# Kernel optimization log

Measured on AMD Instinct MI355X. Metric: run time of the kernel, lower is better.

The kernel has to match this reference:

```python
import jax, jax.numpy as jnp
import numpy as np

N, E, L, S = 20000, 100000, 128, 6   # nodes, edges, latent, message-passing steps
NF, EF, TW, OUT = 11, 5, 5, 1        # node feat, edge feat, time_window, output_size
LN_EPS = 1e-5


def _mlp_ln(x, W1, b1, W2, b2, g, beta):
    # Linear -> ReLU -> Linear -> ReLU -> LayerNorm (matches torch Sequential)
    h = jax.nn.relu(x @ W1 + b1)
    h = jax.nn.relu(h @ W2 + b2)
    mu = h.mean(-1, keepdims=True)
    var = ((h - mu) ** 2).mean(-1, keepdims=True)
    return (h - mu) * jax.lax.rsqrt(var + LN_EPS) * g + beta


def setup_inputs() -> dict:
    key = jax.random.key(0)
    ks = iter(jax.random.split(key, 64))

    def w(shape):
        fan_in = shape[-2]
        return jax.random.normal(next(ks), shape, jnp.float32) / np.float32(np.sqrt(fan_in))

    inp = {
        'node_features': jax.random.normal(next(ks), (1, N, NF), jnp.float32),
        'edge_features': jax.random.normal(next(ks), (1, E, EF), jnp.float32),
        'senders': jax.random.randint(next(ks), (E,), 0, N, jnp.int32),
        'receivers': jax.random.randint(next(ks), (E,), 0, N, jnp.int32),
        'node_mean': jax.random.normal(next(ks), (NF,), jnp.float32),
        'node_std': jnp.ones((NF,), jnp.float32),
        'edge_mean': jax.random.normal(next(ks), (EF,), jnp.float32),
        'edge_std': jnp.ones((EF,), jnp.float32),
        'enc_n_W1': w((NF, L)), 'enc_n_b1': jnp.zeros((L,), jnp.float32),
        'enc_n_W2': w((L, L)), 'enc_n_b2': jnp.zeros((L,), jnp.float32),
        'enc_n_g': jnp.ones((L,), jnp.float32), 'enc_n_beta': jnp.zeros((L,), jnp.float32),
        'enc_e_W1': w((EF, L)), 'enc_e_b1': jnp.zeros((L,), jnp.float32),
        'enc_e_W2': w((L, L)), 'enc_e_b2': jnp.zeros((L,), jnp.float32),
        'enc_e_g': jnp.ones((L,), jnp.float32), 'enc_e_beta': jnp.zeros((L,), jnp.float32),
        'blk_e_W1': w((S, 3 * L, L)), 'blk_e_b1': jnp.zeros((S, L), jnp.float32),
        'blk_e_W2': w((S, L, L)), 'blk_e_b2': jnp.zeros((S, L), jnp.float32),
        'blk_e_g': jnp.ones((S, L), jnp.float32), 'blk_e_beta': jnp.zeros((S, L), jnp.float32),
        'blk_n_W1': w((S, 2 * L, L)), 'blk_n_b1': jnp.zeros((S, L), jnp.float32),
        'blk_n_W2': w((S, L, L)), 'blk_n_b2': jnp.zeros((S, L), jnp.float32),
        'blk_n_g': jnp.ones((S, L), jnp.float32), 'blk_n_beta': jnp.zeros((S, L), jnp.float32),
        'dec_W1': w((L, 8)), 'dec_b1': jnp.zeros((8,), jnp.float32),
        'dec_W2': w((8, TW)), 'dec_b2': jnp.zeros((TW,), jnp.float32),
    }
    return inp


def reference(node_features, edge_features, senders, receivers,
              node_mean, node_std, edge_mean, edge_std,
              enc_n_W1, enc_n_b1, enc_n_W2, enc_n_b2, enc_n_g, enc_n_beta,
              enc_e_W1, enc_e_b1, enc_e_W2, enc_e_b2, enc_e_g, enc_e_beta,
              blk_e_W1, blk_e_b1, blk_e_W2, blk_e_b2, blk_e_g, blk_e_beta,
              blk_n_W1, blk_n_b1, blk_n_W2, blk_n_b2, blk_n_g, blk_n_beta,
              dec_W1, dec_b1, dec_W2, dec_b2):
    # ---- encode (Normalizer in eval mode: (x - mean) / std) ----
    node_lat = _mlp_ln((node_features - node_mean) / node_std,
                       enc_n_W1, enc_n_b1, enc_n_W2, enc_n_b2, enc_n_g, enc_n_beta)  # [1,N,L]
    edge_lat = _mlp_ln((edge_features - edge_mean) / edge_std,
                       enc_e_W1, enc_e_b1, enc_e_W2, enc_e_b2, enc_e_g, enc_e_beta)  # [1,E,L]

    # ---- process: gather -> edge MLP -> scatter_add -> node MLP, residuals ----
    for i in range(S):
        e_in = jnp.concatenate([node_lat[:, senders, :], node_lat[:, receivers, :], edge_lat], axis=-1)  # [1,E,3L]
        new_e = _mlp_ln(e_in, blk_e_W1[i], blk_e_b1[i], blk_e_W2[i], blk_e_b2[i], blk_e_g[i], blk_e_beta[i])
        aggr = jax.ops.segment_sum(new_e[0], receivers, num_segments=N)[None]  # [1,N,L]
        new_n = _mlp_ln(jnp.concatenate([node_lat, aggr], axis=-1),
                        blk_n_W1[i], blk_n_b1[i], blk_n_W2[i], blk_n_b2[i], blk_n_g[i], blk_n_beta[i])
        node_lat = node_lat + new_n
        edge_lat = edge_lat + new_e

    # ---- decode: Conv1d(k=1) == per-node linear; Swish(beta=1) ----
    h = node_lat[0] @ dec_W1 + dec_b1          # [N,8]
    h = h * jax.nn.sigmoid(h)
    dec = h @ dec_W2 + dec_b2                  # [N,TW]
    dt = jnp.repeat(jnp.arange(1, TW + 1), OUT).astype(dec.dtype)  # [TW*OUT]
    delta = (dec * dt).reshape(N, TW, OUT).transpose(1, 0, 2)      # [TW,N,OUT]
    return delta
```

## Files before the change

kernel.cpp:

```cpp
#include <hip/hip_runtime.h>
#include <cstdint>
#include <cstddef>


#define N_NODES 20000
#define N_EDGES 100000
#define LDIM    128
#define NSTEPS  6

typedef float  f32x4  __attribute__((ext_vector_type(4)));
typedef __bf16 bf16x8 __attribute__((ext_vector_type(8)));
typedef __bf16 bf16x2 __attribute__((ext_vector_type(2)));

__device__ __forceinline__ bf16x8 cvt8(const float* p) {
  float4 u = *(const float4*)p;
  float4 v = *(const float4*)(p + 4);
  bf16x8 o;
  o[0] = (__bf16)u.x; o[1] = (__bf16)u.y; o[2] = (__bf16)u.z; o[3] = (__bf16)u.w;
  o[4] = (__bf16)v.x; o[5] = (__bf16)v.y; o[6] = (__bf16)v.z; o[7] = (__bf16)v.w;
  return o;
}

struct PrepArgs {
  const float *s_enW1, *s_enW2, *s_eeW1, *s_eeW2;
  const float *s_beW1, *s_beW2, *s_bnW1, *s_bnW2;
  __bf16 *d_enW1, *d_enW2, *d_eeW1, *d_eeW2;
  __bf16 *d_beW1, *d_beW2, *d_bnW1, *d_bnW2;
  int* counts;
};

__device__ __forceinline__ void swz_src(int idx, int& k, int& col) {
  int j    = idx & 7;
  int lane = (idx >> 3) & 63;
  int ct   = (idx >> 9) & 7;
  int kc   = idx >> 12;
  col = ct * 16 + (lane & 15);
  k   = kc * 32 + (lane >> 4) * 8 + j;
}

__global__ __launch_bounds__(256) void prep_kernel(PrepArgs p) {
  int idx = blockIdx.x * 256 + threadIdx.x;
  int k, col;

  if (idx < 4096) {
    swz_src(idx, k, col);
    p.d_enW1[idx] = (__bf16)((k < 11) ? p.s_enW1[k * 128 + col] : 0.f);
    return;
  }
  idx -= 4096;
  if (idx < 16384) {
    swz_src(idx, k, col);
    p.d_enW2[idx] = (__bf16)p.s_enW2[k * 128 + col];
    return;
  }
  idx -= 16384;
  if (idx < 4096) {
    swz_src(idx, k, col);
    p.d_eeW1[idx] = (__bf16)((k < 5) ? p.s_eeW1[k * 128 + col] : 0.f);
    return;
  }
  idx -= 4096;
  if (idx < 16384) {
    swz_src(idx, k, col);
    p.d_eeW2[idx] = (__bf16)p.s_eeW2[k * 128 + col];
    return;
  }
  idx -= 16384;
  if (idx < 294912) {
    int s = idx / 49152, rem = idx % 49152;
    swz_src(rem, k, col);
    p.d_beW1[idx] = (__bf16)p.s_beW1[(size_t)s * 49152 + k * 128 + col];
    return;
  }
  idx -= 294912;
  if (idx < 98304) {
    int s = idx >> 14, rem = idx & 16383;
    swz_src(rem, k, col);
    p.d_beW2[idx] = (__bf16)p.s_beW2[s * 16384 + k * 128 + col];
    return;
  }
  idx -= 98304;
  if (idx < 196608) {
    int s = idx >> 15, rem = idx & 32767;
    swz_src(rem, k, col);
    p.d_bnW1[idx] = (__bf16)p.s_bnW1[s * 32768 + k * 128 + col];
    return;
  }
  idx -= 196608;
  if (idx < 98304) {
    int s = idx >> 14, rem = idx & 16383;
    swz_src(rem, k, col);
    p.d_bnW2[idx] = (__bf16)p.s_bnW2[s * 16384 + k * 128 + col];
    return;
  }
  idx -= 98304;
  if (idx < N_NODES) p.counts[idx] = 0;
}

__global__ __launch_bounds__(256) void hist_kernel(const int* __restrict__ recv,
                                                   int* __restrict__ counts) {
  int e = blockIdx.x * 256 + threadIdx.x;
  if (e < N_EDGES) atomicAdd(&counts[recv[e]], 1);
}

__global__ __launch_bounds__(1024) void scan_kernel(const int* __restrict__ counts,
                                                    int* __restrict__ row_ptr,
                                                    int* __restrict__ cursor) {
  __shared__ int part[1024];
  const int t = threadIdx.x;
  const int base = t * 20;
  int local[20];
  int s = 0;
#pragma unroll
  for (int i = 0; i < 20; ++i) {
    int idx = base + i;
    int v = (idx < N_NODES) ? counts[idx] : 0;
    local[i] = s;
    s += v;
  }
  part[t] = s;
  __syncthreads();
  for (int off = 1; off < 1024; off <<= 1) {
    int add = (t >= off) ? part[t - off] : 0;
    __syncthreads();
    part[t] += add;
    __syncthreads();
  }
  const int excl = part[t] - s;
#pragma unroll
  for (int i = 0; i < 20; ++i) {
    int idx = base + i;
    if (idx < N_NODES) {
      int v = excl + local[i];
      row_ptr[idx] = v;
      cursor[idx]  = v;
    }
  }
  if (t == 1023) row_ptr[N_NODES] = part[1023];
}

__global__ __launch_bounds__(256) void fill_kernel(const int* __restrict__ recv,
                                                   int* __restrict__ cursor,
                                                   int* __restrict__ edge_list) {
  int e = blockIdx.x * 256 + threadIdx.x;
  if (e < N_EDGES) {
    int r = recv[e];
    int pos = atomicAdd(&cursor[r], 1);
    edge_list[pos] = e;
  }
}

__global__ __launch_bounds__(256) void agg_kernel(
    const int* __restrict__ row_ptr, const int* __restrict__ edge_list,
    const __bf16* __restrict__ new_e, __bf16* __restrict__ aggr_bf) {
  const int wv   = threadIdx.x >> 6;
  const int lane = threadIdx.x & 63;
  const int n    = blockIdx.x * 4 + wv;
  if (n >= N_NODES) return;
  int p = row_ptr[n];
  const int pe = row_ptr[n + 1];
  float s0 = 0.f, s1 = 0.f;
  while (p < pe) {
    const int cnt = min(pe - p, 64);
    int eid = (lane < cnt) ? edge_list[p + lane] : 0;
    for (int j = 0; j < cnt; ++j) {
      const int e = __shfl(eid, j);
      bf16x2 v = *(const bf16x2*)(new_e + (size_t)e * LDIM + lane * 2);
      s0 += (float)v[0];
      s1 += (float)v[1];
    }
    p += cnt;
  }
  bf16x2 o;
  o[0] = (__bf16)s0; o[1] = (__bf16)s1;
  *(bf16x2*)(aggr_bf + (size_t)n * LDIM + lane * 2) = o;
}

struct MlpArgs {
  const float* x; const float* mean; const float* stdv;
  float* node_lat; float* edge_lat;
  __bf16* new_e;
  const __bf16* aggr_bf;
  __bf16* node_bf;
  const int* senders; const int* receivers;
  const __bf16* W1t; const __bf16* W2t;
  const float* b1; const float* b2; const float* g; const float* beta;
  int M;
};

template <int K1, int MODE>
__global__ __launch_bounds__(64, 3) void mlp2_kernel(MlpArgs a) {
  constexpr int NKC = K1 / 32;
  constexpr int RT  = 2;
  constexpr int HS  = 136;

  __shared__ __align__(16) __bf16 H1[32 * HS];

  const int lane  = threadIdx.x & 63;
  const int l15   = lane & 15;
  const int quad  = lane >> 4;
  const int M     = a.M;
  const int rbase = blockIdx.x * 32;

  __bf16* h1w = H1;

  int rowA[RT];
#pragma unroll
  for (int rt = 0; rt < RT; ++rt) {
    int r = rbase + rt * 16 + l15;
    rowA[rt] = (r < M) ? r : (M - 1);
  }

  int sA[RT], rA[RT];
  if constexpr (MODE == 2) {
#pragma unroll
    for (int rt = 0; rt < RT; ++rt) {
      sA[rt] = a.senders[rowA[rt]];
      rA[rt] = a.receivers[rowA[rt]];
    }
  }

  f32x4 acc[RT][8];
#pragma unroll
  for (int rt = 0; rt < RT; ++rt)
#pragma unroll
    for (int i = 0; i < 8; ++i) acc[rt][i] = (f32x4)(0.f);

  if constexpr (MODE == 0 || MODE == 1) {
    constexpr int KIN = (MODE == 0) ? 11 : 5;
    bf16x8 af[RT];
#pragma unroll
    for (int rt = 0; rt < RT; ++rt) {
      const float* xr = a.x + (size_t)rowA[rt] * KIN;
#pragma unroll
      for (int j = 0; j < 8; ++j) {
        int c = quad * 8 + j;
        float v = (c < KIN) ? (xr[c] - a.mean[c]) / a.stdv[c] : 0.f;
        af[rt][j] = (__bf16)v;
      }
    }
    bf16x8 bfv[8];
#pragma unroll
    for (int ct = 0; ct < 8; ++ct)
      bfv[ct] = *(const bf16x8*)(a.W1t + (ct * 64 + lane) * 8);
#pragma unroll
    for (int rt = 0; rt < RT; ++rt)
#pragma unroll
      for (int ct = 0; ct < 8; ++ct)
        acc[rt][ct] = __builtin_amdgcn_mfma_f32_16x16x32_bf16(af[rt], bfv[ct], acc[rt][ct], 0, 0, 0);
  } else {
    constexpr int NPH = NKC / 4;
#pragma unroll
    for (int ph = 0; ph < NPH; ++ph) {
      bf16x8 afr[RT][4];
#pragma unroll
      for (int kk = 0; kk < 4; ++kk) {
#pragma unroll
        for (int rt = 0; rt < RT; ++rt) {
          if constexpr (MODE == 2) {
            if (ph == 0)
              afr[rt][kk] = *(const bf16x8*)(a.node_bf + (size_t)sA[rt] * LDIM + kk * 32 + quad * 8);
            else if (ph == 1)
              afr[rt][kk] = *(const bf16x8*)(a.node_bf + (size_t)rA[rt] * LDIM + kk * 32 + quad * 8);
            else
              afr[rt][kk] = cvt8(a.edge_lat + (size_t)rowA[rt] * LDIM + kk * 32 + quad * 8);
          } else {
            if (ph == 0)
              afr[rt][kk] = *(const bf16x8*)(a.node_bf + (size_t)rowA[rt] * LDIM + kk * 32 + quad * 8);
            else
              afr[rt][kk] = *(const bf16x8*)(a.aggr_bf + (size_t)rowA[rt] * LDIM + kk * 32 + quad * 8);
          }
        }
      }
#pragma unroll
      for (int kk = 0; kk < 4; ++kk) {
        const int kc = ph * 4 + kk;
        bf16x8 bfv[8];
#pragma unroll
        for (int ct = 0; ct < 8; ++ct)
          bfv[ct] = *(const bf16x8*)(a.W1t + ((kc * 8 + ct) * 64 + lane) * 8);
#pragma unroll
        for (int rt = 0; rt < RT; ++rt)
#pragma unroll
          for (int ct = 0; ct < 8; ++ct)
            acc[rt][ct] = __builtin_amdgcn_mfma_f32_16x16x32_bf16(afr[rt][kk], bfv[ct], acc[rt][ct], 0, 0, 0);
      }
    }
  }

#pragma unroll
  for (int ct = 0; ct < 8; ++ct) {
    const float bb = a.b1[ct * 16 + l15];
#pragma unroll
    for (int rt = 0; rt < RT; ++rt)
#pragma unroll
      for (int rr = 0; rr < 4; ++rr) {
        float v = fmaxf(acc[rt][ct][rr] + bb, 0.f);
        h1w[(rt * 16 + quad * 4 + rr) * HS + ct * 16 + l15] = (__bf16)v;
      }
  }

#pragma unroll
  for (int rt = 0; rt < RT; ++rt)
#pragma unroll
    for (int i = 0; i < 8; ++i) acc[rt][i] = (f32x4)(0.f);

#pragma unroll
  for (int kc = 0; kc < 4; ++kc) {
    bf16x8 af[RT];
#pragma unroll
    for (int rt = 0; rt < RT; ++rt)
      af[rt] = *(const bf16x8*)(h1w + (rt * 16 + l15) * HS + kc * 32 + quad * 8);
    bf16x8 bfv[8];
#pragma unroll
    for (int ct = 0; ct < 8; ++ct)
      bfv[ct] = *(const bf16x8*)(a.W2t + ((kc * 8 + ct) * 64 + lane) * 8);
#pragma unroll
    for (int rt = 0; rt < RT; ++rt)
#pragma unroll
      for (int ct = 0; ct < 8; ++ct)
        acc[rt][ct] = __builtin_amdgcn_mfma_f32_16x16x32_bf16(af[rt], bfv[ct], acc[rt][ct], 0, 0, 0);
  }

#pragma unroll
  for (int ct = 0; ct < 8; ++ct) {
    const float bb = a.b2[ct * 16 + l15];
#pragma unroll
    for (int rt = 0; rt < RT; ++rt)
#pragma unroll
      for (int rr = 0; rr < 4; ++rr)
        acc[rt][ct][rr] = fmaxf(acc[rt][ct][rr] + bb, 0.f);
  }

  float mu[RT][4], rs[RT][4];
#pragma unroll
  for (int rt = 0; rt < RT; ++rt)
#pragma unroll
    for (int rr = 0; rr < 4; ++rr) {
      float s = 0.f, s2 = 0.f;
#pragma unroll
      for (int ct = 0; ct < 8; ++ct) { float v = acc[rt][ct][rr]; s += v; s2 += v * v; }
      s  += __shfl_xor(s, 1);  s2 += __shfl_xor(s2, 1);
      s  += __shfl_xor(s, 2);  s2 += __shfl_xor(s2, 2);
      s  += __shfl_xor(s, 4);  s2 += __shfl_xor(s2, 4);
      s  += __shfl_xor(s, 8);  s2 += __shfl_xor(s2, 8);
      float m = s * (1.f / 128.f);
      float var = fmaxf(s2 * (1.f / 128.f) - m * m, 0.f);
      mu[rt][rr] = m; rs[rt][rr] = rsqrtf(var + 1e-5f);
    }

  float gv[8], bev[8];
#pragma unroll
  for (int ct = 0; ct < 8; ++ct) {
    gv[ct]  = a.g[ct * 16 + l15];
    bev[ct] = a.beta[ct * 16 + l15];
  }

#pragma unroll
  for (int rt = 0; rt < RT; ++rt)
#pragma unroll
    for (int rr = 0; rr < 4; ++rr) {
      const int row = rbase + rt * 16 + quad * 4 + rr;
      if (row >= M) continue;
      if constexpr (MODE == 2) {
#pragma unroll
        for (int ct = 0; ct < 8; ++ct) {
          const int col = ct * 16 + l15;
          float y = (acc[rt][ct][rr] - mu[rt][rr]) * rs[rt][rr] * gv[ct] + bev[ct];
          a.edge_lat[(size_t)row * LDIM + col] += y;
          a.new_e[(size_t)row * LDIM + col] = (__bf16)y;
        }
      } else if constexpr (MODE == 3) {
#pragma unroll
        for (int ct = 0; ct < 8; ++ct) {
          const int col = ct * 16 + l15;
          float y = (acc[rt][ct][rr] - mu[rt][rr]) * rs[rt][rr] * gv[ct] + bev[ct];
          float nv = a.node_lat[(size_t)row * LDIM + col] + y;
          a.node_lat[(size_t)row * LDIM + col] = nv;
          a.node_bf[(size_t)row * LDIM + col] = (__bf16)nv;
        }
      } else if constexpr (MODE == 0) {
#pragma unroll
        for (int ct = 0; ct < 8; ++ct) {
          const int col = ct * 16 + l15;
          float y = (acc[rt][ct][rr] - mu[rt][rr]) * rs[rt][rr] * gv[ct] + bev[ct];
          a.node_lat[(size_t)row * LDIM + col] = y;
          a.node_bf[(size_t)row * LDIM + col] = (__bf16)y;
        }
      } else {
#pragma unroll
        for (int ct = 0; ct < 8; ++ct) {
          const int col = ct * 16 + l15;
          float y = (acc[rt][ct][rr] - mu[rt][rr]) * rs[rt][rr] * gv[ct] + bev[ct];
          a.edge_lat[(size_t)row * LDIM + col] = y;
        }
      }
    }
}

__global__ __launch_bounds__(256) void decode_kernel(
    const float* __restrict__ node_lat,
    const float* __restrict__ W1, const float* __restrict__ b1,
    const float* __restrict__ W2, const float* __restrict__ b2,
    float* __restrict__ out) {
  __shared__ float X[64][129];
  const int n0 = blockIdx.x * 64;
  for (int idx = threadIdx.x; idx < 64 * 32; idx += 256) {
    int r = idx >> 5, c4 = idx & 31;
    int n = n0 + r; if (n >= N_NODES) n = N_NODES - 1;
    float4 v = *((const float4*)(node_lat + (size_t)n * 128) + c4);
    X[r][c4 * 4 + 0] = v.x; X[r][c4 * 4 + 1] = v.y;
    X[r][c4 * 4 + 2] = v.z; X[r][c4 * 4 + 3] = v.w;
  }
  __syncthreads();
  const int r = threadIdx.x;
  if (r < 64) {
    const int n = n0 + r;
    if (n < N_NODES) {
      float h[8];
#pragma unroll
      for (int j = 0; j < 8; ++j) h[j] = b1[j];
      for (int k = 0; k < 128; ++k) {
        float xv = X[r][k];
#pragma unroll
        for (int j = 0; j < 8; ++j) h[j] = fmaf(xv, W1[k * 8 + j], h[j]);
      }
#pragma unroll
      for (int j = 0; j < 8; ++j) h[j] = h[j] / (1.f + expf(-h[j]));
#pragma unroll
      for (int t = 0; t < 5; ++t) {
        float d = b2[t];
#pragma unroll
        for (int j = 0; j < 8; ++j) d = fmaf(h[j], W2[j * 5 + t], d);
        out[t * N_NODES + n] = d * (float)(t + 1);
      }
    }
  }
}

extern "C" void kernel_launch(void* const* d_in, const int* in_sizes, int n_in,
                              void* d_out, int out_size, void* d_ws, size_t ws_size,
                              hipStream_t stream) {
  (void)in_sizes; (void)n_in; (void)out_size; (void)ws_size;

  const float* node_features = (const float*)d_in[0];
  const float* edge_features = (const float*)d_in[1];
  const int*   senders       = (const int*)d_in[2];
  const int*   receivers     = (const int*)d_in[3];
  const float* node_mean = (const float*)d_in[4];
  const float* node_std  = (const float*)d_in[5];
  const float* edge_mean = (const float*)d_in[6];
  const float* edge_std  = (const float*)d_in[7];
  const float* enc_n_W1 = (const float*)d_in[8];
  const float* enc_n_b1 = (const float*)d_in[9];
  const float* enc_n_W2 = (const float*)d_in[10];
  const float* enc_n_b2 = (const float*)d_in[11];
  const float* enc_n_g    = (const float*)d_in[12];
  const float* enc_n_beta = (const float*)d_in[13];
  const float* enc_e_W1 = (const float*)d_in[14];
  const float* enc_e_b1 = (const float*)d_in[15];
  const float* enc_e_W2 = (const float*)d_in[16];
  const float* enc_e_b2 = (const float*)d_in[17];
  const float* enc_e_g    = (const float*)d_in[18];
  const float* enc_e_beta = (const float*)d_in[19];
  const float* blk_e_W1 = (const float*)d_in[20];
  const float* blk_e_b1 = (const float*)d_in[21];
  const float* blk_e_W2 = (const float*)d_in[22];
  const float* blk_e_b2 = (const float*)d_in[23];
  const float* blk_e_g    = (const float*)d_in[24];
  const float* blk_e_beta = (const float*)d_in[25];
  const float* blk_n_W1 = (const float*)d_in[26];
  const float* blk_n_b1 = (const float*)d_in[27];
  const float* blk_n_W2 = (const float*)d_in[28];
  const float* blk_n_b2 = (const float*)d_in[29];
  const float* blk_n_g    = (const float*)d_in[30];
  const float* blk_n_beta = (const float*)d_in[31];
  const float* dec_W1 = (const float*)d_in[32];
  const float* dec_b1 = (const float*)d_in[33];
  const float* dec_W2 = (const float*)d_in[34];
  const float* dec_b2 = (const float*)d_in[35];

  char* ws = (char*)d_ws;
  float*  node_lat = (float*)(ws);
  float*  edge_lat = (float*)(ws + 10240000);
  __bf16* new_e    = (__bf16*)(ws + 61440000);
  __bf16* wb       = (__bf16*)(ws + 87040000);
  int* counts    = (int*)(ws + 88498176);
  int* row_ptr   = (int*)(ws + 88578176);
  int* cursor    = (int*)(ws + 88658192);
  int* edge_list = (int*)(ws + 88738192);
  __bf16* aggr_bf = (__bf16*)(ws + 89138192);
  __bf16* node_bf = (__bf16*)(ws + 94258192);

  __bf16* enW1s = wb;
  __bf16* enW2s = enW1s + 4096;
  __bf16* eeW1s = enW2s + 16384;
  __bf16* eeW2s = eeW1s + 4096;
  __bf16* beW1s = eeW2s + 16384;
  __bf16* beW2s = beW1s + 6 * 49152;
  __bf16* bnW1s = beW2s + 6 * 16384;
  __bf16* bnW2s = bnW1s + 6 * 32768;

  PrepArgs pa;
  pa.s_enW1 = enc_n_W1; pa.s_enW2 = enc_n_W2; pa.s_eeW1 = enc_e_W1; pa.s_eeW2 = enc_e_W2;
  pa.s_beW1 = blk_e_W1; pa.s_beW2 = blk_e_W2; pa.s_bnW1 = blk_n_W1; pa.s_bnW2 = blk_n_W2;
  pa.d_enW1 = enW1s; pa.d_enW2 = enW2s; pa.d_eeW1 = eeW1s; pa.d_eeW2 = eeW2s;
  pa.d_beW1 = beW1s; pa.d_beW2 = beW2s; pa.d_bnW1 = bnW1s; pa.d_bnW2 = bnW2s;
  pa.counts = counts;
  prep_kernel<<<2927, 256, 0, stream>>>(pa);

  hist_kernel<<<(N_EDGES + 255) / 256, 256, 0, stream>>>(receivers, counts);
  scan_kernel<<<1, 1024, 0, stream>>>(counts, row_ptr, cursor);
  fill_kernel<<<(N_EDGES + 255) / 256, 256, 0, stream>>>(receivers, cursor, edge_list);

  const int NODE_BLOCKS = (N_NODES + 31) / 32;
  const int EDGE_BLOCKS = (N_EDGES + 31) / 32;
  const int DEC_BLOCKS  = (N_NODES + 63) / 64;
  const int AGG_BLOCKS  = (N_NODES + 3) / 4;

  MlpArgs base;
  base.node_lat = node_lat; base.edge_lat = edge_lat; base.new_e = new_e;
  base.aggr_bf = aggr_bf; base.node_bf = node_bf;
  base.senders = senders; base.receivers = receivers;
  base.x = nullptr; base.mean = nullptr; base.stdv = nullptr;

  {
    MlpArgs a = base;
    a.x = node_features; a.mean = node_mean; a.stdv = node_std;
    a.W1t = enW1s; a.W2t = enW2s;
    a.b1 = enc_n_b1; a.b2 = enc_n_b2; a.g = enc_n_g; a.beta = enc_n_beta;
    a.M = N_NODES;
    mlp2_kernel<32, 0><<<NODE_BLOCKS, 64, 0, stream>>>(a);
  }
  {
    MlpArgs a = base;
    a.x = edge_features; a.mean = edge_mean; a.stdv = edge_std;
    a.W1t = eeW1s; a.W2t = eeW2s;
    a.b1 = enc_e_b1; a.b2 = enc_e_b2; a.g = enc_e_g; a.beta = enc_e_beta;
    a.M = N_EDGES;
    mlp2_kernel<32, 1><<<EDGE_BLOCKS, 64, 0, stream>>>(a);
  }

  for (int i = 0; i < NSTEPS; ++i) {
    {
      MlpArgs a = base;
      a.W1t = beW1s + (size_t)i * 49152; a.W2t = beW2s + (size_t)i * 16384;
      a.b1 = blk_e_b1 + i * 128; a.b2 = blk_e_b2 + i * 128;
      a.g = blk_e_g + i * 128; a.beta = blk_e_beta + i * 128;
      a.M = N_EDGES;
      mlp2_kernel<384, 2><<<EDGE_BLOCKS, 64, 0, stream>>>(a);
    }
    agg_kernel<<<AGG_BLOCKS, 256, 0, stream>>>(row_ptr, edge_list, new_e, aggr_bf);
    {
      MlpArgs a = base;
      a.W1t = bnW1s + (size_t)i * 32768; a.W2t = bnW2s + (size_t)i * 16384;
      a.b1 = blk_n_b1 + i * 128; a.b2 = blk_n_b2 + i * 128;
      a.g = blk_n_g + i * 128; a.beta = blk_n_beta + i * 128;
      a.M = N_NODES;
      mlp2_kernel<256, 3><<<NODE_BLOCKS, 64, 0, stream>>>(a);
    }
  }

  decode_kernel<<<DEC_BLOCKS, 256, 0, stream>>>(
      node_lat, dec_W1, dec_b1, dec_W2, dec_b2, (float*)d_out);
}
```

Before: 705.3 us.

## Precompute per-node sender/receiver projections before edge MLP gather

Splits the edge MLP's first layer so that the sender and receiver slices of W1 are applied once per node by a new projection kernel into an fp32 buffer P. The edge kernel then gathers the projected rows, adds the edge-latent matmul and bias, and applies ReLU, which cuts the per-edge first-layer MFMA work by two thirds. In exchange it gathers fp32 256-wide rows instead of bf16 128-wide rows, staging goes through fp32 shared memory, and each step adds a kernel launch. It also skips the edge_lat residual update on the last step, since that value is never read afterwards.

Measured after the change: 867.1 us. +22.9%, slower.

```diff
diff --git a/kernel.cpp b/kernel.cpp
--- a/kernel.cpp
+++ b/kernel.cpp
@@ -26,6 +26,7 @@
   const float *s_beW1, *s_beW2, *s_bnW1, *s_bnW2;
   __bf16 *d_enW1, *d_enW2, *d_eeW1, *d_eeW2;
   __bf16 *d_beW1, *d_beW2, *d_bnW1, *d_bnW2;
+  __bf16 *d_Wp;
   int* counts;
 };
 
@@ -94,6 +95,21 @@
     return;
   }
   idx -= 98304;
+  if (idx < 196608) {
+    int s = idx >> 15, rem = idx & 32767;
+    int j    = rem & 7;
+    int lane = (rem >> 3) & 63;
+    int ct   = (rem >> 9) & 15;
+    int kc   = rem >> 13;
+    int outcol = ct * 16 + (lane & 15);
+    int kk = kc * 32 + (lane >> 4) * 8 + j;
+    float v = (outcol < 128)
+        ? p.s_beW1[(size_t)s * 49152 + kk * 128 + outcol]
+        : p.s_beW1[(size_t)s * 49152 + (128 + kk) * 128 + (outcol - 128)];
+    p.d_Wp[idx] = (__bf16)v;
+    return;
+  }
+  idx -= 196608;
   if (idx < N_NODES) p.counts[idx] = 0;
 }
 
@@ -176,16 +192,54 @@
   *(bf16x2*)(aggr_bf + (size_t)n * LDIM + lane * 2) = o;
 }
 
+__global__ __launch_bounds__(64, 4) void proj_kernel(
+    const __bf16* __restrict__ node_bf, const __bf16* __restrict__ Wp,
+    float* __restrict__ P) {
+  const int lane = threadIdx.x & 63;
+  const int l15  = lane & 15;
+  const int quad = lane >> 4;
+  const int rbase = blockIdx.x * 16;
+  int row = rbase + l15; if (row >= N_NODES) row = N_NODES - 1;
+
+  bf16x8 af[4];
+#pragma unroll
+  for (int kc = 0; kc < 4; ++kc)
+    af[kc] = *(const bf16x8*)(node_bf + (size_t)row * LDIM + kc * 32 + quad * 8);
+
+  f32x4 acc[16];
+#pragma unroll
+  for (int i = 0; i < 16; ++i) acc[i] = (f32x4)(0.f);
+
+#pragma unroll
+  for (int kc = 0; kc < 4; ++kc)
+#pragma unroll
+    for (int ct = 0; ct < 16; ++ct) {
+      bf16x8 b = *(const bf16x8*)(Wp + ((kc * 16 + ct) * 64 + lane) * 8);
+      acc[ct] = __builtin_amdgcn_mfma_f32_16x16x32_bf16(af[kc], b, acc[ct], 0, 0, 0);
+    }
+
+#pragma unroll
+  for (int ct = 0; ct < 16; ++ct)
+#pragma unroll
+    for (int rr = 0; rr < 4; ++rr) {
+      int r2 = rbase + quad * 4 + rr;
+      if (r2 < N_NODES)
+        P[(size_t)r2 * 256 + ct * 16 + l15] = acc[ct][rr];
+    }
+}
+
 struct MlpArgs {
   const float* x; const float* mean; const float* stdv;
   float* node_lat; float* edge_lat;
   __bf16* new_e;
   const __bf16* aggr_bf;
   __bf16* node_bf;
+  const float* P;
   const int* senders; const int* receivers;
   const __bf16* W1t; const __bf16* W2t;
   const float* b1; const float* b2; const float* g; const float* beta;
   int M;
+  int write_elat;
 };
 
 template <int K1, int MODE>
@@ -193,8 +247,10 @@
   constexpr int NKC = K1 / 32;
   constexpr int RT  = 2;
   constexpr int HS  = 136;
-
-  __shared__ __align__(16) __bf16 H1[32 * HS];
+  constexpr int FS  = 132;
+  constexpr int SMB = (MODE == 2) ? (32 * FS * 4) : (32 * HS * 2);
+
+  __shared__ __align__(16) char SMEM[SMB];
 
   const int lane  = threadIdx.x & 63;
   const int l15   = lane & 15;
@@ -202,8 +258,6 @@
   const int M     = a.M;
   const int rbase = blockIdx.x * 32;
 
-  __bf16* h1w = H1;
-
   int rowA[RT];
 #pragma unroll
   for (int rt = 0; rt < RT; ++rt) {
@@ -226,100 +280,168 @@
 #pragma unroll
     for (int i = 0; i < 8; ++i) acc[rt][i] = (f32x4)(0.f);
 
-  if constexpr (MODE == 0 || MODE == 1) {
-    constexpr int KIN = (MODE == 0) ? 11 : 5;
-    bf16x8 af[RT];
+  if constexpr (MODE == 2) {
+    float* SP = (float*)SMEM;
+    bf16x8 afr[RT][4];
+#pragma unroll
+    for (int kk = 0; kk < 4; ++kk)
+#pragma unroll
+      for (int rt = 0; rt < RT; ++rt)
+        afr[rt][kk] = cvt8(a.edge_lat + (size_t)rowA[rt] * LDIM + kk * 32 + quad * 8);
+#pragma unroll
+    for (int kk = 0; kk < 4; ++kk) {
+      bf16x8 bfv[8];
+#pragma unroll
+      for (int ct = 0; ct < 8; ++ct)
+        bfv[ct] = *(const bf16x8*)(a.W1t + (((kk + 8) * 8 + ct) * 64 + lane) * 8);
+#pragma unroll
+      for (int rt = 0; rt < RT; ++rt)
+#pragma unroll
+        for (int ct = 0; ct < 8; ++ct)
+          acc[rt][ct] = __builtin_amdgcn_mfma_f32_16x16x32_bf16(afr[rt][kk], bfv[ct], acc[rt][ct], 0, 0, 0);
+    }
+#pragma unroll
+    for (int ct = 0; ct < 8; ++ct)
+#pragma unroll
+      for (int rt = 0; rt < RT; ++rt)
+#pragma unroll
+        for (int rr = 0; rr < 4; ++rr)
+          SP[(rt * 16 + quad * 4 + rr) * FS + ct * 16 + l15] = acc[rt][ct][rr];
+
 #pragma unroll
     for (int rt = 0; rt < RT; ++rt) {
-      const float* xr = a.x + (size_t)rowA[rt] * KIN;
-#pragma unroll
-      for (int j = 0; j < 8; ++j) {
-        int c = quad * 8 + j;
-        float v = (c < KIN) ? (xr[c] - a.mean[c]) / a.stdv[c] : 0.f;
-        af[rt][j] = (__bf16)v;
+      const float* Ps = a.P + (size_t)sA[rt] * 256;
+      const float* Pr = a.P + (size_t)rA[rt] * 256 + 128;
+      float* spr = SP + (rt * 16 + l15) * FS;
+#pragma unroll
+      for (int kk = 0; kk < 4; ++kk) {
+        const int c0 = kk * 32 + quad * 8;
+        float4 a0 = *(const float4*)(Ps + c0);
+        float4 a1 = *(const float4*)(Ps + c0 + 4);
+        float4 b0 = *(const float4*)(Pr + c0);
+        float4 b1v = *(const float4*)(Pr + c0 + 4);
+        float4 g0 = *(const float4*)(a.b1 + c0);
+        float4 g1 = *(const float4*)(a.b1 + c0 + 4);
+        float4 c0v = *(const float4*)(spr + c0);
+        float4 c1v = *(const float4*)(spr + c0 + 4);
+        c0v.x = fmaxf(c0v.x + a0.x + b0.x + g0.x, 0.f);
+        c0v.y = fmaxf(c0v.y + a0.y + b0.y + g0.y, 0.f);
+        c0v.z = fmaxf(c0v.z + a0.z + b0.z + g0.z, 0.f);
+        c0v.w = fmaxf(c0v.w + a0.w + b0.w + g0.w, 0.f);
+        c1v.x = fmaxf(c1v.x + a1.x + b1v.x + g1.x, 0.f);
+        c1v.y = fmaxf(c1v.y + a1.y + b1v.y + g1.y, 0.f);
+        c1v.z = fmaxf(c1v.z + a1.z + b1v.z + g1.z, 0.f);
+        c1v.w = fmaxf(c1v.w + a1.w + b1v.w + g1.w, 0.f);
+        *(float4*)(spr + c0)     = c0v;
+        *(float4*)(spr + c0 + 4) = c1v;
       }
     }
-    bf16x8 bfv[8];
-#pragma unroll
-    for (int ct = 0; ct < 8; ++ct)
-      bfv[ct] = *(const bf16x8*)(a.W1t + (ct * 64 + lane) * 8);
+
 #pragma unroll
     for (int rt = 0; rt < RT; ++rt)
 #pragma unroll
+      for (int i = 0; i < 8; ++i) acc[rt][i] = (f32x4)(0.f);
+#pragma unroll
+    for (int kc = 0; kc < 4; ++kc) {
+      bf16x8 af2[RT];
+#pragma unroll
+      for (int rt = 0; rt < RT; ++rt)
+        af2[rt] = cvt8(SP + (rt * 16 + l15) * FS + kc * 32 + quad * 8);
+      bf16x8 bfv[8];
+#pragma unroll
       for (int ct = 0; ct < 8; ++ct)
-        acc[rt][ct] = __builtin_amdgcn_mfma_f32_16x16x32_bf16(af[rt], bfv[ct], acc[rt][ct], 0, 0, 0);
+        bfv[ct] = *(const bf16x8*)(a.W2t + ((kc * 8 + ct) * 64 + lane) * 8);
+#pragma unroll
+      for (int rt = 0; rt < RT; ++rt)
+#pragma unroll
+        for (int ct = 0; ct < 8; ++ct)
+          acc[rt][ct] = __builtin_amdgcn_mfma_f32_16x16x32_bf16(af2[rt], bfv[ct], acc[rt][ct], 0, 0, 0);
+    }
   } else {
-    constexpr int NPH = NKC / 4;
-#pragma unroll
-    for (int ph = 0; ph < NPH; ++ph) {
-      bf16x8 afr[RT][4];
-#pragma unroll
-      for (int kk = 0; kk < 4; ++kk) {
-#pragma unroll
-        for (int rt = 0; rt < RT; ++rt) {
-          if constexpr (MODE == 2) {
-            if (ph == 0)
-              afr[rt][kk] = *(const bf16x8*)(a.node_bf + (size_t)sA[rt] * LDIM + kk * 32 + quad * 8);
-            else if (ph == 1)
-              afr[rt][kk] = *(const bf16x8*)(a.node_bf + (size_t)rA[rt] * LDIM + kk * 32 + quad * 8);
-            else
-              afr[rt][kk] = cvt8(a.edge_lat + (size_t)rowA[rt] * LDIM + kk * 32 + quad * 8);
-          } else {
-            if (ph == 0)
-              afr[rt][kk] = *(const bf16x8*)(a.node_bf + (size_t)rowA[rt] * LDIM + kk * 32 + quad * 8);
-            else
-              afr[rt][kk] = *(const bf16x8*)(a.aggr_bf + (size_t)rowA[rt] * LDIM + kk * 32 + quad * 8);
-          }
+    __bf16* h1w = (__bf16*)SMEM;
+    if constexpr (MODE == 0 || MODE == 1) {
+      constexpr int KIN = (MODE == 0) ? 11 : 5;
+      bf16x8 af[RT];
+#pragma unroll
+      for (int rt = 0; rt < RT; ++rt) {
+        const float* xr = a.x + (size_t)rowA[rt] * KIN;
+#pragma unroll
+        for (int j = 0; j < 8; ++j) {
+          int c = quad * 8 + j;
+          float v = (c < KIN) ? (xr[c] - a.mean[c]) / a.stdv[c] : 0.f;
+          af[rt][j] = (__bf16)v;
         }
       }
-#pragma unroll
-      for (int kk = 0; kk < 4; ++kk) {
-        const int kc = ph * 4 + kk;
-        bf16x8 bfv[8];
+      bf16x8 bfv[8];
+#pragma unroll
+      for (int ct = 0; ct < 8; ++ct)
+        bfv[ct] = *(const bf16x8*)(a.W1t + (ct * 64 + lane) * 8);
+#pragma unroll
+      for (int rt = 0; rt < RT; ++rt)
 #pragma unroll
         for (int ct = 0; ct < 8; ++ct)
-          bfv[ct] = *(const bf16x8*)(a.W1t + ((kc * 8 + ct) * 64 + lane) * 8);
-#pragma unroll
-        for (int rt = 0; rt < RT; ++rt)
+          acc[rt][ct] = __builtin_amdgcn_mfma_f32_16x16x32_bf16(af[rt], bfv[ct], acc[rt][ct], 0, 0, 0);
+    } else {
+      constexpr int NPH = NKC / 4;
+#pragma unroll
+      for (int ph = 0; ph < NPH; ++ph) {
+        bf16x8 afr[RT][4];
+#pragma unroll
+        for (int kk = 0; kk < 4; ++kk)
+#pragma unroll
+          for (int rt = 0; rt < RT; ++rt) {
+            const __bf16* src = (ph == 0) ? (a.node_bf + (size_t)rowA[rt] * LDIM)
+                                          : (a.aggr_bf + (size_t)rowA[rt] * LDIM);
+            afr[rt][kk] = *(const bf16x8*)(src + kk * 32 + quad * 8);
+          }
+#pragma unroll
+        for (int kk = 0; kk < 4; ++kk) {
+          const int kc = ph * 4 + kk;
+          bf16x8 bfv[8];
 #pragma unroll
           for (int ct = 0; ct < 8; ++ct)
-            acc[rt][ct] = __builtin_amdgcn_mfma_f32_16x16x32_bf16(afr[rt][kk], bfv[ct], acc[rt][ct], 0, 0, 0);
+            bfv[ct] = *(const bf16x8*)(a.W1t + ((kc * 8 + ct) * 64 + lane) * 8);
+#pragma unroll
+          for (int rt = 0; rt < RT; ++rt)
+#pragma unroll
+            for (int ct = 0; ct < 8; ++ct)
+              acc[rt][ct] = __builtin_amdgcn_mfma_f32_16x16x32_bf16(afr[rt][kk], bfv[ct], acc[rt][ct], 0, 0, 0);
+        }
       }
     }
-  }
-
-#pragma unroll
-  for (int ct = 0; ct < 8; ++ct) {
-    const float bb = a.b1[ct * 16 + l15];
+
+#pragma unroll
+    for (int ct = 0; ct < 8; ++ct) {
+      const float bb = a.b1[ct * 16 + l15];
+#pragma unroll
+      for (int rt = 0; rt < RT; ++rt)
+#pragma unroll
+        for (int rr = 0; rr < 4; ++rr) {
+          float v = fmaxf(acc[rt][ct][rr] + bb, 0.f);
+          h1w[(rt * 16 + quad * 4 + rr) * HS + ct * 16 + l15] = (__bf16)v;
+        }
+    }
+
 #pragma unroll
     for (int rt = 0; rt < RT; ++rt)
 #pragma unroll
-      for (int rr = 0; rr < 4; ++rr) {
-        float v = fmaxf(acc[rt][ct][rr] + bb, 0.f);
-        h1w[(rt * 16 + quad * 4 + rr) * HS + ct * 16 + l15] = (__bf16)v;
-      }
-  }
-
-#pragma unroll
-  for (int rt = 0; rt < RT; ++rt)
-#pragma unroll
-    for (int i = 0; i < 8; ++i) acc[rt][i] = (f32x4)(0.f);
-
-#pragma unroll
-  for (int kc = 0; kc < 4; ++kc) {
-    bf16x8 af[RT];
-#pragma unroll
-    for (int rt = 0; rt < RT; ++rt)
-      af[rt] = *(const bf16x8*)(h1w + (rt * 16 + l15) * HS + kc * 32 + quad * 8);
-    bf16x8 bfv[8];
-#pragma unroll
-    for (int ct = 0; ct < 8; ++ct)
-      bfv[ct] = *(const bf16x8*)(a.W2t + ((kc * 8 + ct) * 64 + lane) * 8);
-#pragma unroll
-    for (int rt = 0; rt < RT; ++rt)
+      for (int i = 0; i < 8; ++i) acc[rt][i] = (f32x4)(0.f);
+#pragma unroll
+    for (int kc = 0; kc < 4; ++kc) {
+      bf16x8 af[RT];
+#pragma unroll
+      for (int rt = 0; rt < RT; ++rt)
+        af[rt] = *(const bf16x8*)(h1w + (rt * 16 + l15) * HS + kc * 32 + quad * 8);
+      bf16x8 bfv[8];
 #pragma unroll
       for (int ct = 0; ct < 8; ++ct)
-        acc[rt][ct] = __builtin_amdgcn_mfma_f32_16x16x32_bf16(af[rt], bfv[ct], acc[rt][ct], 0, 0, 0);
+        bfv[ct] = *(const bf16x8*)(a.W2t + ((kc * 8 + ct) * 64 + lane) * 8);
+#pragma unroll
+      for (int rt = 0; rt < RT; ++rt)
+#pragma unroll
+        for (int ct = 0; ct < 8; ++ct)
+          acc[rt][ct] = __builtin_amdgcn_mfma_f32_16x16x32_bf16(af[rt], bfv[ct], acc[rt][ct], 0, 0, 0);
+    }
   }
 
 #pragma unroll
@@ -367,7 +489,8 @@
         for (int ct = 0; ct < 8; ++ct) {
           const int col = ct * 16 + l15;
           float y = (acc[rt][ct][rr] - mu[rt][rr]) * rs[rt][rr] * gv[ct] + bev[ct];
-          a.edge_lat[(size_t)row * LDIM + col] += y;
+          if (a.write_elat)
+            a.edge_lat[(size_t)row * LDIM + col] += y;
           a.new_e[(size_t)row * LDIM + col] = (__bf16)y;
         }
       } else if constexpr (MODE == 3) {
@@ -491,6 +614,8 @@
   int* edge_list = (int*)(ws + 88738192);
   __bf16* aggr_bf = (__bf16*)(ws + 89138192);
   __bf16* node_bf = (__bf16*)(ws + 94258192);
+  float*  Pbuf    = (float*)(ws + 99378192);
+  __bf16* Wp      = (__bf16*)(ws + 119858192);
 
   __bf16* enW1s = wb;
   __bf16* enW2s = enW1s + 4096;
@@ -506,8 +631,9 @@
   pa.s_beW1 = blk_e_W1; pa.s_beW2 = blk_e_W2; pa.s_bnW1 = blk_n_W1; pa.s_bnW2 = blk_n_W2;
   pa.d_enW1 = enW1s; pa.d_enW2 = enW2s; pa.d_eeW1 = eeW1s; pa.d_eeW2 = eeW2s;
   pa.d_beW1 = beW1s; pa.d_beW2 = beW2s; pa.d_bnW1 = bnW1s; pa.d_bnW2 = bnW2s;
+  pa.d_Wp = Wp;
   pa.counts = counts;
-  prep_kernel<<<2927, 256, 0, stream>>>(pa);
+  prep_kernel<<<3695, 256, 0, stream>>>(pa);
 
   hist_kernel<<<(N_EDGES + 255) / 256, 256, 0, stream>>>(receivers, counts);
   scan_kernel<<<1, 1024, 0, stream>>>(counts, row_ptr, cursor);
@@ -517,12 +643,14 @@
   const int EDGE_BLOCKS = (N_EDGES + 31) / 32;
   const int DEC_BLOCKS  = (N_NODES + 63) / 64;
   const int AGG_BLOCKS  = (N_NODES + 3) / 4;
+  const int PROJ_BLOCKS = (N_NODES + 15) / 16;
 
   MlpArgs base;
   base.node_lat = node_lat; base.edge_lat = edge_lat; base.new_e = new_e;
-  base.aggr_bf = aggr_bf; base.node_bf = node_bf;
+  base.aggr_bf = aggr_bf; base.node_bf = node_bf; base.P = Pbuf;
   base.senders = senders; base.receivers = receivers;
   base.x = nullptr; base.mean = nullptr; base.stdv = nullptr;
+  base.write_elat = 1;
 
   {
     MlpArgs a = base;
@@ -542,12 +670,14 @@
   }
 
   for (int i = 0; i < NSTEPS; ++i) {
+    proj_kernel<<<PROJ_BLOCKS, 64, 0, stream>>>(node_bf, Wp + (size_t)i * 32768, Pbuf);
     {
       MlpArgs a = base;
       a.W1t = beW1s + (size_t)i * 49152; a.W2t = beW2s + (size_t)i * 16384;
       a.b1 = blk_e_b1 + i * 128; a.b2 = blk_e_b2 + i * 128;
       a.g = blk_e_g + i * 128; a.beta = blk_e_beta + i * 128;
       a.M = N_EDGES;
+      a.write_elat = (i < NSTEPS - 1) ? 1 : 0;
       mlp2_kernel<384, 2><<<EDGE_BLOCKS, 64, 0, stream>>>(a);
     }
     agg_kernel<<<AGG_BLOCKS, 256, 0, stream>>>(row_ptr, edge_list, new_e, aggr_bf);
```

## Store edges in receiver-sorted order and skip final edge latent update

Applied to the files above, without the earlier changes.

Edges are permuted into CSR order by receiver: the fill kernel writes permuted sender and receiver arrays, the edge encoder reads features through the permutation, and every edge MLP works in sorted order. The aggregation kernel can then read contiguous new_e rows without indirection through edge_list. The edge MLP also no longer writes edge_lat on the last step, since nothing reads it afterwards. Order within each receiver depends on atomics, so summation order is nondeterministic, which is harmless for the result.

Result: slower. 731.6 us (+3.7%).

```diff
diff --git a/kernel.cpp b/kernel.cpp
--- a/kernel.cpp
+++ b/kernel.cpp
@@ -139,19 +139,22 @@
   if (t == 1023) row_ptr[N_NODES] = part[1023];
 }
 
-__global__ __launch_bounds__(256) void fill_kernel(const int* __restrict__ recv,
-                                                   int* __restrict__ cursor,
-                                                   int* __restrict__ edge_list) {
+__global__ __launch_bounds__(256) void fill_kernel(
+    const int* __restrict__ send, const int* __restrict__ recv,
+    int* __restrict__ cursor, int* __restrict__ edge_list,
+    int* __restrict__ sp, int* __restrict__ rp) {
   int e = blockIdx.x * 256 + threadIdx.x;
   if (e < N_EDGES) {
     int r = recv[e];
     int pos = atomicAdd(&cursor[r], 1);
     edge_list[pos] = e;
+    sp[pos] = send[e];
+    rp[pos] = r;
   }
 }
 
 __global__ __launch_bounds__(256) void agg_kernel(
-    const int* __restrict__ row_ptr, const int* __restrict__ edge_list,
+    const int* __restrict__ row_ptr,
     const __bf16* __restrict__ new_e, __bf16* __restrict__ aggr_bf) {
   const int wv   = threadIdx.x >> 6;
   const int lane = threadIdx.x & 63;
@@ -160,16 +163,18 @@
   int p = row_ptr[n];
   const int pe = row_ptr[n + 1];
   float s0 = 0.f, s1 = 0.f;
-  while (p < pe) {
-    const int cnt = min(pe - p, 64);
-    int eid = (lane < cnt) ? edge_list[p + lane] : 0;
-    for (int j = 0; j < cnt; ++j) {
-      const int e = __shfl(eid, j);
-      bf16x2 v = *(const bf16x2*)(new_e + (size_t)e * LDIM + lane * 2);
-      s0 += (float)v[0];
-      s1 += (float)v[1];
-    }
-    p += cnt;
+  for (; p + 4 <= pe; p += 4) {
+    bf16x2 v0 = *(const bf16x2*)(new_e + (size_t)(p + 0) * LDIM + lane * 2);
+    bf16x2 v1 = *(const bf16x2*)(new_e + (size_t)(p + 1) * LDIM + lane * 2);
+    bf16x2 v2 = *(const bf16x2*)(new_e + (size_t)(p + 2) * LDIM + lane * 2);
+    bf16x2 v3 = *(const bf16x2*)(new_e + (size_t)(p + 3) * LDIM + lane * 2);
+    s0 += (float)v0[0] + (float)v1[0] + (float)v2[0] + (float)v3[0];
+    s1 += (float)v0[1] + (float)v1[1] + (float)v2[1] + (float)v3[1];
+  }
+  for (; p < pe; ++p) {
+    bf16x2 v = *(const bf16x2*)(new_e + (size_t)p * LDIM + lane * 2);
+    s0 += (float)v[0];
+    s1 += (float)v[1];
   }
   bf16x2 o;
   o[0] = (__bf16)s0; o[1] = (__bf16)s1;
@@ -182,10 +187,11 @@
   __bf16* new_e;
   const __bf16* aggr_bf;
   __bf16* node_bf;
-  const int* senders; const int* receivers;
+  const int* sp; const int* rp; const int* eperm;
   const __bf16* W1t; const __bf16* W2t;
   const float* b1; const float* b2; const float* g; const float* beta;
   int M;
+  int write_elat;
 };
 
 template <int K1, int MODE>
@@ -215,8 +221,8 @@
   if constexpr (MODE == 2) {
 #pragma unroll
     for (int rt = 0; rt < RT; ++rt) {
-      sA[rt] = a.senders[rowA[rt]];
-      rA[rt] = a.receivers[rowA[rt]];
+      sA[rt] = a.sp[rowA[rt]];
+      rA[rt] = a.rp[rowA[rt]];
     }
   }
 
@@ -231,7 +237,9 @@
     bf16x8 af[RT];
 #pragma unroll
     for (int rt = 0; rt < RT; ++rt) {
-      const float* xr = a.x + (size_t)rowA[rt] * KIN;
+      int orig = rowA[rt];
+      if constexpr (MODE == 1) orig = a.eperm[rowA[rt]];
+      const float* xr = a.x + (size_t)orig * KIN;
 #pragma unroll
       for (int j = 0; j < 8; ++j) {
         int c = quad * 8 + j;
@@ -367,7 +375,8 @@
         for (int ct = 0; ct < 8; ++ct) {
           const int col = ct * 16 + l15;
           float y = (acc[rt][ct][rr] - mu[rt][rr]) * rs[rt][rr] * gv[ct] + bev[ct];
-          a.edge_lat[(size_t)row * LDIM + col] += y;
+          if (a.write_elat)
+            a.edge_lat[(size_t)row * LDIM + col] += y;
           a.new_e[(size_t)row * LDIM + col] = (__bf16)y;
         }
       } else if constexpr (MODE == 3) {
@@ -491,6 +500,8 @@
   int* edge_list = (int*)(ws + 88738192);
   __bf16* aggr_bf = (__bf16*)(ws + 89138192);
   __bf16* node_bf = (__bf16*)(ws + 94258192);
+  int* sp        = (int*)(ws + 99378192);
+  int* rp        = (int*)(ws + 99778192);
 
   __bf16* enW1s = wb;
   __bf16* enW2s = enW1s + 4096;
@@ -511,7 +522,8 @@
 
   hist_kernel<<<(N_EDGES + 255) / 256, 256, 0, stream>>>(receivers, counts);
   scan_kernel<<<1, 1024, 0, stream>>>(counts, row_ptr, cursor);
-  fill_kernel<<<(N_EDGES + 255) / 256, 256, 0, stream>>>(receivers, cursor, edge_list);
+  fill_kernel<<<(N_EDGES + 255) / 256, 256, 0, stream>>>(senders, receivers,
+                                                         cursor, edge_list, sp, rp);
 
   const int NODE_BLOCKS = (N_NODES + 31) / 32;
   const int EDGE_BLOCKS = (N_EDGES + 31) / 32;
@@ -521,8 +533,9 @@
   MlpArgs base;
   base.node_lat = node_lat; base.edge_lat = edge_lat; base.new_e = new_e;
   base.aggr_bf = aggr_bf; base.node_bf = node_bf;
-  base.senders = senders; base.receivers = receivers;
+  base.sp = sp; base.rp = rp; base.eperm = edge_list;
   base.x = nullptr; base.mean = nullptr; base.stdv = nullptr;
+  base.write_elat = 1;
 
   {
     MlpArgs a = base;
@@ -548,9 +561,10 @@
       a.b1 = blk_e_b1 + i * 128; a.b2 = blk_e_b2 + i * 128;
       a.g = blk_e_g + i * 128; a.beta = blk_e_beta + i * 128;
       a.M = N_EDGES;
+      a.write_elat = (i < NSTEPS - 1) ? 1 : 0;
       mlp2_kernel<384, 2><<<EDGE_BLOCKS, 64, 0, stream>>>(a);
     }
-    agg_kernel<<<AGG_BLOCKS, 256, 0, stream>>>(row_ptr, edge_list, new_e, aggr_bf);
+    agg_kernel<<<AGG_BLOCKS, 256, 0, stream>>>(row_ptr, new_e, aggr_bf);
     {
       MlpArgs a = base;
       a.W1t = bnW1s + (size_t)i * 32768; a.W2t = bnW2s + (size_t)i * 16384;
```
